# Kernel optimization log

Hardware: AMD Instinct MI355X
Metric: run time of the kernel (lower is better)

## Reference

```python
import jax, jax.numpy as jnp
import numpy as np

MOMENTUM = 0.9
NUM_CLASSES = 10000
BANK_DIM = 1024
BATCH = 4096


def setup_inputs() -> dict:
    key = jax.random.key(0)
    k1, k2, k3, k4 = jax.random.split(key, 4)
    scores = jax.random.normal(k1, (BATCH, NUM_CLASSES), dtype=jnp.float32)
    feat = jax.random.normal(k2, (BATCH, BANK_DIM), dtype=jnp.float32)
    update_feat_bank = jax.random.normal(k3, (NUM_CLASSES, BANK_DIM), dtype=jnp.float32)
    update_times = jnp.zeros((NUM_CLASSES,), dtype=jnp.float32)
    labels = jax.random.randint(k4, (BATCH,), 0, NUM_CLASSES, dtype=jnp.int64 if jax.config.read('jax_enable_x64') else jnp.int32)
    return {"scores": scores, "feat": feat, "update_feat_bank": update_feat_bank,
            "update_times": update_times, "labels": labels}


def reference(scores, feat, update_feat_bank, update_times, labels):
    """Faithful vectorization of AvgMem.proc with choose='err'.

    Original (sequential, per chosen sample i in batch order):
        bank[l_i] = m * bank[l_i] + (1 - m) * feat[i];  times[l_i] += 1
    Closed form per label l with chosen samples i1<...<ik:
        bank[l] = m^k * bank0[l] + (1-m) * sum_j m^(k-j) feat[i_j]
    i.e. each sample's weight is (1-m) * m^(#later chosen samples with same label).
    """
    m = jnp.float32(MOMENTUM)
    C = update_feat_bank.shape[0]
    B = labels.shape[0]

    # softmax is monotonic -> argmax of softmax(scores) == argmax of scores
    pred = jnp.argmax(scores, axis=1)
    chosen = pred != labels  # choose == 'err'

    # c[i] = number of later chosen samples with the same label (BxB pairwise)
    same = labels[:, None] == labels[None, :]
    later = jnp.arange(B)[None, :] > jnp.arange(B)[:, None]
    c = jnp.sum(same & later & chosen[None, :], axis=1).astype(feat.dtype)

    w = jnp.where(chosen, (1.0 - m) * m ** c, 0.0).astype(feat.dtype)  # [B]

    delta = jax.ops.segment_sum(w[:, None] * feat, labels, num_segments=C)  # [C, D]
    k = jax.ops.segment_sum(chosen.astype(update_times.dtype), labels, num_segments=C)  # [C]

    new_bank = (m ** k)[:, None] * update_feat_bank + delta
    new_times = update_times + k
    return new_bank, new_times
```

## Files before the change

### kernel.cpp

```cpp
#include <hip/hip_runtime.h>

#define MOM 0.9f
#define ONE_MINUS_MOM 0.1f
#define MAXK 16

typedef float f32x4 __attribute__((ext_vector_type(4)));

__global__ __launch_bounds__(256) void argmax_scatter_kernel(
    const float* __restrict__ scores, const int* __restrict__ labels,
    int* __restrict__ cnt, int* __restrict__ slot, int C)
{
    const int row = blockIdx.x;
    const float* rp = scores + (size_t)row * C;
    const int nv = C >> 2;
    const float4* r4 = (const float4*)rp;

    float b0 = -__builtin_inff(), b1 = b0, b2 = b0, b3 = b0;
    int v0 = 0x7fffffff, v1 = v0, v2 = v0, v3 = v0;
    for (int v = threadIdx.x; v < nv; v += 256) {
        float4 s = r4[v];
        if (s.x > b0) { b0 = s.x; v0 = v; }
        if (s.y > b1) { b1 = s.y; v1 = v; }
        if (s.z > b2) { b2 = s.z; v2 = v; }
        if (s.w > b3) { b3 = s.w; v3 = v; }
    }
    float best = b0; int bidx = (v0 << 2) | 0;
    { int oi = (v1 << 2) | 1; if (b1 > best || (b1 == best && oi < bidx)) { best = b1; bidx = oi; } }
    { int oi = (v2 << 2) | 2; if (b2 > best || (b2 == best && oi < bidx)) { best = b2; bidx = oi; } }
    { int oi = (v3 << 2) | 3; if (b3 > best || (b3 == best && oi < bidx)) { best = b3; bidx = oi; } }
    for (int c = (nv << 2) + threadIdx.x; c < C; c += 256) {
        float s = rp[c];
        if (s > best) { best = s; bidx = c; }
    }

    #pragma unroll
    for (int off = 32; off > 0; off >>= 1) {
        float ov = __shfl_xor(best, off);
        int   oi = __shfl_xor(bidx, off);
        if (ov > best || (ov == best && oi < bidx)) { best = ov; bidx = oi; }
    }

    __shared__ float sv[4];
    __shared__ int   si[4];
    const int lane = threadIdx.x & 63;
    const int wid  = threadIdx.x >> 6;
    if (lane == 0) { sv[wid] = best; si[wid] = bidx; }
    __syncthreads();
    if (threadIdx.x == 0) {
        float bv = sv[0]; int bi = si[0];
        #pragma unroll
        for (int w = 1; w < 4; ++w) {
            float ov = sv[w]; int oi = si[w];
            if (ov > bv || (ov == bv && oi < bi)) { bv = ov; bi = oi; }
        }
        int lab = labels[row];
        if (bi != lab) {
            int pos = atomicAdd(&cnt[lab], 1);
            if (pos < MAXK) slot[lab * MAXK + pos] = row;
        }
    }
}

__global__ __launch_bounds__(256) void update_kernel(
    const float* __restrict__ bank, const float* __restrict__ times,
    const float* __restrict__ feat, const int* __restrict__ cnt,
    const int* __restrict__ slot,
    float* __restrict__ out_bank, float* __restrict__ out_times, int C, int D)
{
    const int lane = threadIdx.x & 63;
    const int wid  = threadIdx.x >> 6;
    const int l = (blockIdx.x << 2) | wid;
    if (l >= C) return;

    const float4* brow = (const float4*)(bank + (size_t)l * D);
    float4* orow = (float4*)(out_bank + (size_t)l * D);
    const int nv = D >> 2;
    const int sbase = l * MAXK;

    if (nv == 256) {
        float4 a0 = brow[lane];
        float4 a1 = brow[lane + 64];
        float4 a2 = brow[lane + 128];
        float4 a3 = brow[lane + 192];
        const float tl = times[l];
        const int k = cnt[l];
        const int kk = (k < MAXK) ? k : MAXK;

        float scale = 1.0f;
        const int kc = (k < 128) ? k : 128;
        for (int p = 0; p < kc; ++p) scale *= MOM;
        a0.x *= scale; a0.y *= scale; a0.z *= scale; a0.w *= scale;
        a1.x *= scale; a1.y *= scale; a1.z *= scale; a1.w *= scale;
        a2.x *= scale; a2.y *= scale; a2.z *= scale; a2.w *= scale;
        a3.x *= scale; a3.y *= scale; a3.z *= scale; a3.w *= scale;

        int last = -1;
        for (int s = 0; s < kk; ++s) {
            int cur = 0x7fffffff;
            for (int p = 0; p < kk; ++p) {
                int j = slot[sbase + p];
                if (j > last && j < cur) cur = j;
            }
            int e = k - 1 - s; if (e > 127) e = 127;
            float w = ONE_MINUS_MOM;
            for (int t = 0; t < e; ++t) w *= MOM;

            const float4* f4 = (const float4*)(feat + (size_t)cur * D);
            float4 f0 = f4[lane];
            float4 f1 = f4[lane + 64];
            float4 f2 = f4[lane + 128];
            float4 f3 = f4[lane + 192];
            a0.x += w * f0.x; a0.y += w * f0.y; a0.z += w * f0.z; a0.w += w * f0.w;
            a1.x += w * f1.x; a1.y += w * f1.y; a1.z += w * f1.z; a1.w += w * f1.w;
            a2.x += w * f2.x; a2.y += w * f2.y; a2.z += w * f2.z; a2.w += w * f2.w;
            a3.x += w * f3.x; a3.y += w * f3.y; a3.z += w * f3.z; a3.w += w * f3.w;
            last = cur;
        }
        orow[lane] = a0;
        orow[lane + 64] = a1;
        orow[lane + 128] = a2;
        orow[lane + 192] = a3;
        if (lane == 0) out_times[l] = tl + (float)k;
    } else {
        const float tl = times[l];
        const int k = cnt[l];
        const int kk = (k < MAXK) ? k : MAXK;
        float scale = 1.0f;
        const int kc = (k < 128) ? k : 128;
        for (int p = 0; p < kc; ++p) scale *= MOM;
        for (int v = lane; v < nv; v += 64) {
            float4 a = brow[v];
            a.x *= scale; a.y *= scale; a.z *= scale; a.w *= scale;
            int last = -1;
            for (int s = 0; s < kk; ++s) {
                int cur = 0x7fffffff;
                for (int p = 0; p < kk; ++p) {
                    int j = slot[sbase + p];
                    if (j > last && j < cur) cur = j;
                }
                int e = k - 1 - s; if (e > 127) e = 127;
                float w = ONE_MINUS_MOM;
                for (int t = 0; t < e; ++t) w *= MOM;
                const float4* f4 = (const float4*)(feat + (size_t)cur * D);
                float4 f = f4[v];
                a.x += w * f.x; a.y += w * f.y; a.z += w * f.z; a.w += w * f.w;
                last = cur;
            }
            orow[v] = a;
        }
        if (lane == 0) out_times[l] = tl + (float)k;
    }
}

extern "C" void kernel_launch(void* const* d_in, const int* in_sizes, int n_in,
                              void* d_out, int out_size, void* d_ws, size_t ws_size,
                              hipStream_t stream) {
    const float* scores = (const float*)d_in[0];
    const float* feat   = (const float*)d_in[1];
    const float* bank   = (const float*)d_in[2];
    const float* times  = (const float*)d_in[3];
    const int*   labels = (const int*)d_in[4];

    const int B = in_sizes[4];
    const int C = in_sizes[3];
    const int D = in_sizes[1] / B;

    float* out_bank  = (float*)d_out;
    float* out_times = out_bank + (size_t)C * D;

    int* cnt  = (int*)d_ws;
    int* slot = cnt + C;

    hipMemsetAsync(cnt, 0, (size_t)C * sizeof(int), stream);
    argmax_scatter_kernel<<<B, 256, 0, stream>>>(scores, labels, cnt, slot, C);
    update_kernel<<<(C + 3) / 4, 256, 0, stream>>>(bank, times, feat, cnt, slot,
                                                   out_bank, out_times, C, D);
}
```

Measured before the change: 55.60 us.

## Replace global atomic scatter and memset with per-block key scan in shared memory

The argmax kernel now writes one packed key per row (label and an error flag) instead of doing a global atomicAdd into per-label slot lists. That removes the memset of the count array. Each update block scans the whole key array and builds its own 4-label lists in shared memory with shared atomics. This drops one launch and the global atomics, but every one of about 2500 blocks now reads all 4096 keys (16KB, mostly served from cache). The bank row loads are issued before the scan so they can overlap with it.

```diff
diff --git a/kernel.cpp b/kernel.cpp
--- a/kernel.cpp
+++ b/kernel.cpp
@@ -4,11 +4,9 @@
 #define ONE_MINUS_MOM 0.1f
 #define MAXK 16
 
-typedef float f32x4 __attribute__((ext_vector_type(4)));
-
-__global__ __launch_bounds__(256) void argmax_scatter_kernel(
+__global__ __launch_bounds__(256) void argmax_key_kernel(
     const float* __restrict__ scores, const int* __restrict__ labels,
-    int* __restrict__ cnt, int* __restrict__ slot, int C)
+    int* __restrict__ key, int C)
 {
     const int row = blockIdx.x;
     const float* rp = scores + (size_t)row * C;
@@ -54,41 +52,90 @@
             if (ov > bv || (ov == bv && oi < bi)) { bv = ov; bi = oi; }
         }
         int lab = labels[row];
-        if (bi != lab) {
-            int pos = atomicAdd(&cnt[lab], 1);
-            if (pos < MAXK) slot[lab * MAXK + pos] = row;
-        }
+        key[row] = (lab << 1) | ((bi != lab) ? 1 : 0);
     }
 }
 
 __global__ __launch_bounds__(256) void update_kernel(
     const float* __restrict__ bank, const float* __restrict__ times,
-    const float* __restrict__ feat, const int* __restrict__ cnt,
-    const int* __restrict__ slot,
-    float* __restrict__ out_bank, float* __restrict__ out_times, int C, int D)
+    const float* __restrict__ feat, const int* __restrict__ key,
+    float* __restrict__ out_bank, float* __restrict__ out_times,
+    int B, int C, int D)
 {
-    const int lane = threadIdx.x & 63;
-    const int wid  = threadIdx.x >> 6;
-    const int l = (blockIdx.x << 2) | wid;
-    if (l >= C) return;
-
-    const float4* brow = (const float4*)(bank + (size_t)l * D);
-    float4* orow = (float4*)(out_bank + (size_t)l * D);
+    const int tid  = threadIdx.x;
+    const int lane = tid & 63;
+    const int wid  = tid >> 6;
+    const int lbase = (int)blockIdx.x << 2;
+    const int l = lbase | wid;
+
+    __shared__ int scnt[4];
+    __shared__ int list[4][MAXK];
+
+    const bool valid = (l < C);
+    const float4* brow = valid ? (const float4*)(bank + (size_t)l * D) : nullptr;
+    float4* orow = valid ? (float4*)(out_bank + (size_t)l * D) : nullptr;
     const int nv = D >> 2;
-    const int sbase = l * MAXK;
-
-    if (nv == 256) {
-        float4 a0 = brow[lane];
-        float4 a1 = brow[lane + 64];
-        float4 a2 = brow[lane + 128];
-        float4 a3 = brow[lane + 192];
-        const float tl = times[l];
-        const int k = cnt[l];
-        const int kk = (k < MAXK) ? k : MAXK;
-
-        float scale = 1.0f;
-        const int kc = (k < 128) ? k : 128;
-        for (int p = 0; p < kc; ++p) scale *= MOM;
+
+    float4 a0, a1, a2, a3;
+    float tl = 0.0f;
+    const bool fast = (nv == 256) && valid;
+    if (fast) {
+        a0 = brow[lane];
+        a1 = brow[lane + 64];
+        a2 = brow[lane + 128];
+        a3 = brow[lane + 192];
+        tl = times[l];
+    }
+
+    if (tid < 4) scnt[tid] = 0;
+    __syncthreads();
+
+    const int nk4 = B >> 2;
+    const int4* k4 = (const int4*)key;
+    for (int q = tid; q < nk4; q += 256) {
+        int4 kv = k4[q];
+        int j0 = q << 2;
+        int c0 = (kv.x >> 1) - lbase;
+        if ((kv.x & 1) && (unsigned)c0 < 4u) {
+            int pos = atomicAdd(&scnt[c0], 1);
+            if (pos < MAXK) list[c0][pos] = j0;
+        }
+        int c1 = (kv.y >> 1) - lbase;
+        if ((kv.y & 1) && (unsigned)c1 < 4u) {
+            int pos = atomicAdd(&scnt[c1], 1);
+            if (pos < MAXK) list[c1][pos] = j0 + 1;
+        }
+        int c2 = (kv.z >> 1) - lbase;
+        if ((kv.z & 1) && (unsigned)c2 < 4u) {
+            int pos = atomicAdd(&scnt[c2], 1);
+            if (pos < MAXK) list[c2][pos] = j0 + 2;
+        }
+        int c3 = (kv.w >> 1) - lbase;
+        if ((kv.w & 1) && (unsigned)c3 < 4u) {
+            int pos = atomicAdd(&scnt[c3], 1);
+            if (pos < MAXK) list[c3][pos] = j0 + 3;
+        }
+    }
+    for (int j = (nk4 << 2) + tid; j < B; j += 256) {
+        int kj = key[j];
+        int c = (kj >> 1) - lbase;
+        if ((kj & 1) && (unsigned)c < 4u) {
+            int pos = atomicAdd(&scnt[c], 1);
+            if (pos < MAXK) list[c][pos] = j;
+        }
+    }
+    __syncthreads();
+
+    if (!valid) return;
+
+    const int k = scnt[wid];
+    const int kk = (k < MAXK) ? k : MAXK;
+
+    float scale = 1.0f;
+    const int kc = (k < 128) ? k : 128;
+    for (int p = 0; p < kc; ++p) scale *= MOM;
+
+    if (fast) {
         a0.x *= scale; a0.y *= scale; a0.z *= scale; a0.w *= scale;
         a1.x *= scale; a1.y *= scale; a1.z *= scale; a1.w *= scale;
         a2.x *= scale; a2.y *= scale; a2.z *= scale; a2.w *= scale;
@@ -98,7 +145,7 @@
         for (int s = 0; s < kk; ++s) {
             int cur = 0x7fffffff;
             for (int p = 0; p < kk; ++p) {
-                int j = slot[sbase + p];
+                int j = list[wid][p];
                 if (j > last && j < cur) cur = j;
             }
             int e = k - 1 - s; if (e > 127) e = 127;
@@ -122,12 +169,7 @@
         orow[lane + 192] = a3;
         if (lane == 0) out_times[l] = tl + (float)k;
     } else {
-        const float tl = times[l];
-        const int k = cnt[l];
-        const int kk = (k < MAXK) ? k : MAXK;
-        float scale = 1.0f;
-        const int kc = (k < 128) ? k : 128;
-        for (int p = 0; p < kc; ++p) scale *= MOM;
+        const float tlg = times[l];
         for (int v = lane; v < nv; v += 64) {
             float4 a = brow[v];
             a.x *= scale; a.y *= scale; a.z *= scale; a.w *= scale;
@@ -135,7 +177,7 @@
             for (int s = 0; s < kk; ++s) {
                 int cur = 0x7fffffff;
                 for (int p = 0; p < kk; ++p) {
-                    int j = slot[sbase + p];
+                    int j = list[wid][p];
                     if (j > last && j < cur) cur = j;
                 }
                 int e = k - 1 - s; if (e > 127) e = 127;
@@ -148,7 +190,7 @@
             }
             orow[v] = a;
         }
-        if (lane == 0) out_times[l] = tl + (float)k;
+        if (lane == 0) out_times[l] = tlg + (float)k;
     }
 }
 
@@ -168,11 +210,9 @@
     float* out_bank  = (float*)d_out;
     float* out_times = out_bank + (size_t)C * D;
 
-    int* cnt  = (int*)d_ws;
-    int* slot = cnt + C;
-
-    hipMemsetAsync(cnt, 0, (size_t)C * sizeof(int), stream);
-    argmax_scatter_kernel<<<B, 256, 0, stream>>>(scores, labels, cnt, slot, C);
-    update_kernel<<<(C + 3) / 4, 256, 0, stream>>>(bank, times, feat, cnt, slot,
-                                                   out_bank, out_times, C, D);
+    int* key = (int*)d_ws;
+
+    argmax_key_kernel<<<B, 256, 0, stream>>>(scores, labels, key, C);
+    update_kernel<<<(C + 3) / 4, 256, 0, stream>>>(bank, times, feat, key,
+                                                   out_bank, out_times, B, C, D);
 }
```

After: 50.65 us. 8.9% less time.
